# Kernel tuning notes

Hardware: AMD Instinct MI355X
Metric: run time of the kernel (lower is better)

Reference implementation:

```python
import jax, jax.numpy as jnp
import numpy as np

DISTANCE_SCALE = 25.0
VIEW_PE = 6
STEP = 0.02  # nominal ray-march step size used to scale dists


def positional_encoding(positions, freqs):
    # matches torch: (positions[..., None] * 2**k).reshape(..., freqs*C) -> [sin, cos]
    freq_bands = 2.0 ** jnp.arange(freqs, dtype=positions.dtype)
    pts = (positions[..., None] * freq_bands).reshape(positions.shape[:-1] + (freqs * positions.shape[-1],))
    return jnp.concatenate([jnp.sin(pts), jnp.cos(pts)], axis=-1)


def setup_inputs() -> dict:
    key = jax.random.key(0)
    ks = jax.random.split(key, 10)
    n_rays, n_samples, C, featureC = 4096, 256, 27, 128
    in_mlpC = 3 + 2 * VIEW_PE * 3 + C  # 66
    density_features = jax.random.normal(ks[0], (n_rays, n_samples), jnp.float32)
    app_features = jax.random.normal(ks[1], (n_rays, n_samples, C), jnp.float32)
    viewdirs = jax.random.normal(ks[2], (n_rays, 3), jnp.float32)
    viewdirs = viewdirs / jnp.linalg.norm(viewdirs, axis=-1, keepdims=True)
    dists = jax.random.uniform(ks[3], (n_rays, n_samples), jnp.float32) * STEP
    s1 = 1.0 / np.sqrt(in_mlpC)
    s2 = 1.0 / np.sqrt(featureC)
    W1 = jax.random.uniform(ks[4], (in_mlpC, featureC), jnp.float32, -s1, s1)
    b1 = jax.random.uniform(ks[5], (featureC,), jnp.float32, -s1, s1)
    W2 = jax.random.uniform(ks[6], (featureC, featureC), jnp.float32, -s2, s2)
    b2 = jax.random.uniform(ks[7], (featureC,), jnp.float32, -s2, s2)
    W3 = jax.random.uniform(ks[8], (featureC, 3), jnp.float32, -s2, s2)
    b3 = jnp.zeros((3,), jnp.float32)  # torch init: constant_(bias, 0)
    return {"density_features": density_features, "app_features": app_features,
            "viewdirs": viewdirs, "dists": dists,
            "W1": W1, "b1": b1, "W2": W2, "b2": b2, "W3": W3, "b3": b3}


def reference(density_features, app_features, viewdirs, dists, W1, b1, W2, b2, W3, b3):
    # feature2density (relu activation)
    sigma = jax.nn.relu(density_features)  # [R, S]
    # raw2alpha
    alpha = 1.0 - jnp.exp(-sigma * dists * DISTANCE_SCALE)  # [R, S]
    T = jnp.cumprod(jnp.concatenate([jnp.ones((alpha.shape[0], 1), alpha.dtype),
                                     1.0 - alpha + 1e-10], axis=-1), axis=-1)
    weights = alpha * T[:, :-1]  # [R, S]
    # radiance MLP over all sample points
    R, S, C = app_features.shape
    vd = jnp.broadcast_to(viewdirs[:, None, :], (R, S, 3))
    mlp_in = jnp.concatenate([app_features, vd, positional_encoding(vd, VIEW_PE)], axis=-1)  # [R,S,66]
    h = jax.nn.relu(mlp_in @ W1 + b1)
    h = jax.nn.relu(h @ W2 + b2)
    rgb = jax.nn.sigmoid(h @ W3 + b3)  # [R, S, 3]
    # composite (white background)
    acc_map = jnp.sum(weights, axis=-1)  # [R]
    rgb_map = jnp.einsum('rs,rsc->rc', weights, rgb)  # [R, 3]
    rgb_map = jnp.clip(rgb_map + (1.0 - acc_map[:, None]), 0.0, 1.0)
    return rgb_map
```

## Files before the change

### kernel.cpp

```cpp
#include <hip/hip_runtime.h>
#include <hip/hip_bf16.h>

typedef float f32x4 __attribute__((ext_vector_type(4)));
typedef short s16x8 __attribute__((ext_vector_type(8)));
typedef unsigned int u32;
typedef u32 u32x2 __attribute__((ext_vector_type(2)));

#define DIST_SCALE 25.0f

__device__ __forceinline__ unsigned short f2b(float f) {
  union { float f; unsigned u; } v; v.f = f;
  unsigned r = v.u + 0x7fffu + ((v.u >> 16) & 1u);
  return (unsigned short)(r >> 16);
}

__device__ __forceinline__ u32 cvtpk(float lo, float hi) {
  u32 r;
  asm("v_cvt_pk_bf16_f32 %0, %1, %2" : "=v"(r) : "v"(lo), "v"(hi));
  return r;
}

__device__ __forceinline__ int swzH(int s, int chbyte) {
  return (s * 256 + chbyte) ^ ((s & 7) << 4);
}

__global__ void prep_weights(const float* __restrict__ W1, const float* __restrict__ W2,
                             const float* __restrict__ W3, unsigned short* __restrict__ ws) {
  int t = blockIdx.x * 256 + threadIdx.x;
  int stride = gridDim.x * 256;
  for (int i = t; i < 128 * 32; i += stride) {
    int n = i >> 5, k = i & 31;
    ws[i] = (k < 27) ? f2b(W1[k * 128 + n]) : (unsigned short)0;
  }
  unsigned short* w2t = ws + 4096;
  for (int i = t; i < 128 * 128; i += stride) {
    int n = i >> 7, k = i & 127;
    w2t[i] = f2b(W2[k * 128 + n]);
  }
  unsigned short* w3p = ws + 4096 + 16384;
  for (int i = t; i < 4 * 16 * 32; i += stride) {
    int wv = i >> 9, rem = i & 511, n = rem >> 5, ks = rem & 31;
    int kg = ks >> 3, j = ks & 7;
    int ch = wv * 32 + ((j >> 2) << 4) + kg * 4 + (j & 3);
    w3p[i] = (n < 3) ? f2b(W3[ch * 3 + n]) : (unsigned short)0;
  }
}

__global__ void __launch_bounds__(256, 3) nerf_main(
    const float* __restrict__ dens, const float* __restrict__ app,
    const float* __restrict__ vdirs, const float* __restrict__ dists,
    const float* __restrict__ W1, const float* __restrict__ b1,
    const float* __restrict__ b2v, const float* __restrict__ b3v,
    const unsigned short* __restrict__ wsb, float* __restrict__ out) {
  __shared__ unsigned short Xs[64 * 40];
  __shared__ unsigned short HA[64 * 128];
  __shared__ float part[4 * 64 * 3];
  __shared__ float wbuf[256];
  __shared__ float hcbuf[128];
  __shared__ float featbuf[40];
  __shared__ float red[4][4];

  const int t = threadIdx.x;
  const int lane = t & 63;
  const int wv = t >> 6;
  const int r = blockIdx.x;

  const unsigned short* W1aT = wsb;
  const unsigned short* W2T = wsb + 4096;
  const unsigned short* W3P = wsb + 4096 + 16384;
  char* HAb = (char*)HA;

  const int cl = lane & 15;
  const int kg = lane >> 4;
  const int chBase = wv * 32;

  for (int i = t; i < 1280; i += 256) ((u32*)Xs)[i] = 0u;
  if (t < 39) {
    float val;
    if (t < 3) val = vdirs[r * 3 + t];
    else {
      int jj = t - 3;
      int trig = jj / 18;
      int rem = jj % 18;
      int c = rem / 6, k = rem % 6;
      float v = vdirs[r * 3 + c] * (float)(1 << k);
      val = trig ? cosf(v) : sinf(v);
    }
    featbuf[t] = val;
  }
  if (wv == 0) {
    const float4 dv = *(const float4*)(dens + (size_t)r * 256 + lane * 4);
    const float4 tv = *(const float4*)(dists + (size_t)r * 256 + lane * 4);
    float f[4], al[4];
    float dl[4] = {dv.x, dv.y, dv.z, dv.w};
    float tl[4] = {tv.x, tv.y, tv.z, tv.w};
    float p = 1.0f;
#pragma unroll
    for (int q = 0; q < 4; ++q) {
      float sg = fmaxf(dl[q], 0.0f);
      float e = __expf(-sg * tl[q] * DIST_SCALE);
      al[q] = 1.0f - e;
      f[q] = e + 1e-10f;
      p *= f[q];
    }
    float P = p;
#pragma unroll
    for (int dlt = 1; dlt < 64; dlt <<= 1) {
      float v = __shfl_up(P, dlt, 64);
      if (lane >= dlt) P *= v;
    }
    float E = __shfl_up(P, 1, 64);
    if (lane == 0) E = 1.0f;
    float tr = E;
#pragma unroll
    for (int q = 0; q < 4; ++q) { wbuf[lane * 4 + q] = al[q] * tr; tr *= f[q]; }
  }
  __syncthreads();
  if (t < 128) {
    float s = b1[t];
    for (int j = 0; j < 39; ++j) s += featbuf[j] * W1[(27 + j) * 128 + t];
    hcbuf[t] = s;
  }

  s16x8 w1f[2], w2f[2][4], w3s;
#pragma unroll
  for (int nt = 0; nt < 2; ++nt)
    w1f[nt] = *(const s16x8*)(W1aT + (chBase + nt * 16 + cl) * 32 + kg * 8);
#pragma unroll
  for (int nt = 0; nt < 2; ++nt)
#pragma unroll
    for (int kk = 0; kk < 4; ++kk)
      w2f[nt][kk] = *(const s16x8*)(W2T + (chBase + nt * 16 + cl) * 128 + kk * 32 + kg * 8);
  w3s = *(const s16x8*)(W3P + wv * 512 + cl * 32 + kg * 8);

  __syncthreads();

  float pr = 0.0f, pg = 0.0f, pb = 0.0f, pw = 0.0f;
  const float b30 = b3v[0], b31 = b3v[1], b32 = b3v[2];
  const f32x4 hc0 = *(const f32x4*)(hcbuf + chBase + kg * 4);
  const f32x4 hc1 = *(const f32x4*)(hcbuf + chBase + 16 + kg * 4);
  const f32x4 bb0 = *(const f32x4*)(b2v + chBase + kg * 4);
  const f32x4 bb1 = *(const f32x4*)(b2v + chBase + 16 + kg * 4);

  const float* rayBase = app + (size_t)r * 256 * 27;
  f32x4 L0 = *(const f32x4*)(rayBase + 4 * t);
  f32x4 L1 = {};
  if (t < 176) L1 = *(const f32x4*)(rayBase + 4 * (t + 256));

  for (int chunk = 0; chunk < 4; ++chunk) {
    const int sBase = chunk * 64;
    {
      unsigned e0 = 4u * (unsigned)t;
      unsigned s0 = e0 / 27u, c0 = e0 - s0 * 27u;
      unsigned base = s0 * 80u + 2u * c0;
#pragma unroll
      for (int u2 = 0; u2 < 4; ++u2) {
        unsigned a = base + 2u * u2 + ((c0 + u2 >= 27u) ? 26u : 0u);
        *(unsigned short*)((char*)Xs + a) = f2b(L0[u2]);
      }
      if (t < 176) {
        unsigned e1 = 4u * (unsigned)(t + 256);
        unsigned s1 = e1 / 27u, c1 = e1 - s1 * 27u;
        unsigned bs1 = s1 * 80u + 2u * c1;
#pragma unroll
        for (int u2 = 0; u2 < 4; ++u2) {
          unsigned a = bs1 + 2u * u2 + ((c1 + u2 >= 27u) ? 26u : 0u);
          *(unsigned short*)((char*)Xs + a) = f2b(L1[u2]);
        }
      }
    }
    __syncthreads();

    if (chunk < 3) {
      const float* slab = rayBase + (size_t)(chunk + 1) * 1728;
      L0 = *(const f32x4*)(slab + 4 * t);
      if (t < 176) L1 = *(const f32x4*)(slab + 4 * (t + 256));
    }

#pragma unroll
    for (int st = 0; st < 4; ++st) {
      const int s = st * 16 + cl;
      s16x8 xb = *(const s16x8*)((char*)Xs + s * 80 + kg * 16);
      f32x4 a0 = hc0, a1 = hc1;
      a0 = __builtin_amdgcn_mfma_f32_16x16x32_bf16(w1f[0], xb, a0, 0, 0, 0);
      a1 = __builtin_amdgcn_mfma_f32_16x16x32_bf16(w1f[1], xb, a1, 0, 0, 0);
      u32x2 pk0 = {cvtpk(fmaxf(a0[0], 0.0f), fmaxf(a0[1], 0.0f)),
                   cvtpk(fmaxf(a0[2], 0.0f), fmaxf(a0[3], 0.0f))};
      u32x2 pk1 = {cvtpk(fmaxf(a1[0], 0.0f), fmaxf(a1[1], 0.0f)),
                   cvtpk(fmaxf(a1[2], 0.0f), fmaxf(a1[3], 0.0f))};
      *(u32x2*)(HAb + swzH(s, (chBase + kg * 4) * 2)) = pk0;
      *(u32x2*)(HAb + swzH(s, (chBase + 16 + kg * 4) * 2)) = pk1;
    }
    __syncthreads();

#pragma unroll
    for (int st = 0; st < 4; ++st) {
      const int s = st * 16 + cl;
      s16x8 hbf[4];
#pragma unroll
      for (int kk = 0; kk < 4; ++kk)
        hbf[kk] = *(const s16x8*)(HAb + swzH(s, (kk * 32 + kg * 8) * 2));
      f32x4 a0 = bb0, a1 = bb1;
#pragma unroll
      for (int kk = 0; kk < 4; ++kk) {
        a0 = __builtin_amdgcn_mfma_f32_16x16x32_bf16(w2f[0][kk], hbf[kk], a0, 0, 0, 0);
        a1 = __builtin_amdgcn_mfma_f32_16x16x32_bf16(w2f[1][kk], hbf[kk], a1, 0, 0, 0);
      }
      union { u32 u[4]; s16x8 v; } b3;
      b3.u[0] = cvtpk(fmaxf(a0[0], 0.0f), fmaxf(a0[1], 0.0f));
      b3.u[1] = cvtpk(fmaxf(a0[2], 0.0f), fmaxf(a0[3], 0.0f));
      b3.u[2] = cvtpk(fmaxf(a1[0], 0.0f), fmaxf(a1[1], 0.0f));
      b3.u[3] = cvtpk(fmaxf(a1[2], 0.0f), fmaxf(a1[3], 0.0f));
      f32x4 p3 = {};
      p3 = __builtin_amdgcn_mfma_f32_16x16x32_bf16(w3s, b3.v, p3, 0, 0, 0);
      if (kg == 0) {
        float* pp = part + (wv * 64 + s) * 3;
        pp[0] = p3[0]; pp[1] = p3[1]; pp[2] = p3[2];
      }
    }
    __syncthreads();

    {
      const float* pp = part + ((kg * 64) + wv * 16 + cl) * 3;
      float v0 = pp[0], v1 = pp[1], v2 = pp[2];
      v0 += __shfl_xor(v0, 16, 64); v0 += __shfl_xor(v0, 32, 64);
      v1 += __shfl_xor(v1, 16, 64); v1 += __shfl_xor(v1, 32, 64);
      v2 += __shfl_xor(v2, 16, 64); v2 += __shfl_xor(v2, 32, 64);
      if (kg == 0) {
        float w = wbuf[sBase + wv * 16 + cl];
        pw += w;
        pr += w / (1.0f + __expf(-(v0 + b30)));
        pg += w / (1.0f + __expf(-(v1 + b31)));
        pb += w / (1.0f + __expf(-(v2 + b32)));
      }
    }
  }

  if (kg == 0) {
#pragma unroll
    for (int d = 1; d < 16; d <<= 1) {
      pr += __shfl_xor(pr, d, 64);
      pg += __shfl_xor(pg, d, 64);
      pb += __shfl_xor(pb, d, 64);
      pw += __shfl_xor(pw, d, 64);
    }
    if (lane == 0) { red[wv][0] = pr; red[wv][1] = pg; red[wv][2] = pb; red[wv][3] = pw; }
  }
  __syncthreads();
  if (t == 0) {
    float R = 0, G = 0, B = 0, W = 0;
#pragma unroll
    for (int w = 0; w < 4; ++w) { R += red[w][0]; G += red[w][1]; B += red[w][2]; W += red[w][3]; }
    float bg = 1.0f - W;
    out[r * 3 + 0] = fminf(fmaxf(R + bg, 0.0f), 1.0f);
    out[r * 3 + 1] = fminf(fmaxf(G + bg, 0.0f), 1.0f);
    out[r * 3 + 2] = fminf(fmaxf(B + bg, 0.0f), 1.0f);
  }
}

extern "C" void kernel_launch(void* const* d_in, const int* in_sizes, int n_in,
                              void* d_out, int out_size, void* d_ws, size_t ws_size,
                              hipStream_t stream) {
  const float* dens = (const float*)d_in[0];
  const float* app  = (const float*)d_in[1];
  const float* vd   = (const float*)d_in[2];
  const float* dist = (const float*)d_in[3];
  const float* W1   = (const float*)d_in[4];
  const float* b1   = (const float*)d_in[5];
  const float* W2   = (const float*)d_in[6];
  const float* b2   = (const float*)d_in[7];
  const float* W3   = (const float*)d_in[8];
  const float* b3   = (const float*)d_in[9];
  unsigned short* wsb = (unsigned short*)d_ws;

  prep_weights<<<32, 256, 0, stream>>>(W1, W2, W3, wsb);
  nerf_main<<<4096, 256, 0, stream>>>(dens, app, vd, dist, W1, b1, b2, b3, wsb, (float*)d_out);
}
```

Baseline: 81.67 us.

## Load app features straight into MFMA fragments and fold epilogue reduction across lanes

Drops the LDS staging buffer for the per-chunk app feature slab. Each lane now reads its 8 floats directly from global memory and packs them to bf16 in registers for the first-layer MFMA. This removes one barrier per chunk and the scattered 16-bit LDS stores. Lanes reading past channel 27 pick up values from the next sample, which assumes the padded W1 rows are zero; the last ray's final chunk gets a guard to avoid reading out of bounds. The epilogue is also reorganised so the four lane groups each handle one of R, G, B and the weight sum, with a transposed partial buffer, and LDS is merged into a smaller pool. The explicit next-chunk prefetch is gone, so global load latency now sits directly ahead of the MFMAs.

```diff
diff --git a/kernel.cpp b/kernel.cpp
--- a/kernel.cpp
+++ b/kernel.cpp
@@ -52,12 +52,9 @@
     const float* __restrict__ W1, const float* __restrict__ b1,
     const float* __restrict__ b2v, const float* __restrict__ b3v,
     const unsigned short* __restrict__ wsb, float* __restrict__ out) {
-  __shared__ unsigned short Xs[64 * 40];
   __shared__ unsigned short HA[64 * 128];
-  __shared__ float part[4 * 64 * 3];
+  __shared__ __align__(16) float pool[768];
   __shared__ float wbuf[256];
-  __shared__ float hcbuf[128];
-  __shared__ float featbuf[40];
   __shared__ float red[4][4];
 
   const int t = threadIdx.x;
@@ -73,8 +70,9 @@
   const int cl = lane & 15;
   const int kg = lane >> 4;
   const int chBase = wv * 32;
-
-  for (int i = t; i < 1280; i += 256) ((u32*)Xs)[i] = 0u;
+  float* featbuf = pool;
+  float* hcbuf = pool + 64;
+
   if (t < 39) {
     float val;
     if (t < 3) val = vdirs[r * 3 + t];
@@ -134,56 +132,46 @@
   w3s = *(const s16x8*)(W3P + wv * 512 + cl * 32 + kg * 8);
 
   __syncthreads();
-
-  float pr = 0.0f, pg = 0.0f, pb = 0.0f, pw = 0.0f;
-  const float b30 = b3v[0], b31 = b3v[1], b32 = b3v[2];
   const f32x4 hc0 = *(const f32x4*)(hcbuf + chBase + kg * 4);
   const f32x4 hc1 = *(const f32x4*)(hcbuf + chBase + 16 + kg * 4);
   const f32x4 bb0 = *(const f32x4*)(b2v + chBase + kg * 4);
   const f32x4 bb1 = *(const f32x4*)(b2v + chBase + 16 + kg * 4);
-
-  const float* rayBase = app + (size_t)r * 256 * 27;
-  f32x4 L0 = *(const f32x4*)(rayBase + 4 * t);
-  f32x4 L1 = {};
-  if (t < 176) L1 = *(const f32x4*)(rayBase + 4 * (t + 256));
+  const float b3c = (kg < 3) ? b3v[kg] : 0.0f;
+  float pacc = 0.0f;
+  float* part = pool;
+
+  const float* rayBase = app + (size_t)r * 6912;
 
   for (int chunk = 0; chunk < 4; ++chunk) {
     const int sBase = chunk * 64;
-    {
-      unsigned e0 = 4u * (unsigned)t;
-      unsigned s0 = e0 / 27u, c0 = e0 - s0 * 27u;
-      unsigned base = s0 * 80u + 2u * c0;
-#pragma unroll
-      for (int u2 = 0; u2 < 4; ++u2) {
-        unsigned a = base + 2u * u2 + ((c0 + u2 >= 27u) ? 26u : 0u);
-        *(unsigned short*)((char*)Xs + a) = f2b(L0[u2]);
-      }
-      if (t < 176) {
-        unsigned e1 = 4u * (unsigned)(t + 256);
-        unsigned s1 = e1 / 27u, c1 = e1 - s1 * 27u;
-        unsigned bs1 = s1 * 80u + 2u * c1;
-#pragma unroll
-        for (int u2 = 0; u2 < 4; ++u2) {
-          unsigned a = bs1 + 2u * u2 + ((c1 + u2 >= 27u) ? 26u : 0u);
-          *(unsigned short*)((char*)Xs + a) = f2b(L1[u2]);
-        }
-      }
-    }
-    __syncthreads();
-
-    if (chunk < 3) {
-      const float* slab = rayBase + (size_t)(chunk + 1) * 1728;
-      L0 = *(const f32x4*)(slab + 4 * t);
-      if (t < 176) L1 = *(const f32x4*)(slab + 4 * (t + 256));
-    }
+    const float* ckBase = rayBase + chunk * 1728;
+    const bool tailCk = (r == 4095) && (chunk == 3);
 
 #pragma unroll
     for (int st = 0; st < 4; ++st) {
       const int s = st * 16 + cl;
-      s16x8 xb = *(const s16x8*)((char*)Xs + s * 80 + kg * 16);
+      const float* gp = ckBase + s * 27 + kg * 8;
+      f32x4 va, vb;
+      if (__builtin_expect(tailCk && st == 3, 0)) {
+        if (kg == 3 && cl == 15) {
+          va = (f32x4){gp[0], gp[1], gp[2], 0.0f};
+          vb = (f32x4){0.0f, 0.0f, 0.0f, 0.0f};
+        } else {
+          va = *(const f32x4*)gp;
+          vb = *(const f32x4*)(gp + 4);
+        }
+      } else {
+        va = *(const f32x4*)gp;
+        vb = *(const f32x4*)(gp + 4);
+      }
+      union { u32 u[4]; s16x8 v; } xb;
+      xb.u[0] = cvtpk(va[0], va[1]);
+      xb.u[1] = cvtpk(va[2], va[3]);
+      xb.u[2] = cvtpk(vb[0], vb[1]);
+      xb.u[3] = cvtpk(vb[2], vb[3]);
       f32x4 a0 = hc0, a1 = hc1;
-      a0 = __builtin_amdgcn_mfma_f32_16x16x32_bf16(w1f[0], xb, a0, 0, 0, 0);
-      a1 = __builtin_amdgcn_mfma_f32_16x16x32_bf16(w1f[1], xb, a1, 0, 0, 0);
+      a0 = __builtin_amdgcn_mfma_f32_16x16x32_bf16(w1f[0], xb.v, a0, 0, 0, 0);
+      a1 = __builtin_amdgcn_mfma_f32_16x16x32_bf16(w1f[1], xb.v, a1, 0, 0, 0);
       u32x2 pk0 = {cvtpk(fmaxf(a0[0], 0.0f), fmaxf(a0[1], 0.0f)),
                    cvtpk(fmaxf(a0[2], 0.0f), fmaxf(a0[3], 0.0f))};
       u32x2 pk1 = {cvtpk(fmaxf(a1[0], 0.0f), fmaxf(a1[1], 0.0f)),
@@ -214,43 +202,36 @@
       f32x4 p3 = {};
       p3 = __builtin_amdgcn_mfma_f32_16x16x32_bf16(w3s, b3.v, p3, 0, 0, 0);
       if (kg == 0) {
-        float* pp = part + (wv * 64 + s) * 3;
-        pp[0] = p3[0]; pp[1] = p3[1]; pp[2] = p3[2];
+        float* pp = part + s * 12;
+        pp[wv] = p3[0];
+        pp[4 + wv] = p3[1];
+        pp[8 + wv] = p3[2];
       }
     }
     __syncthreads();
 
     {
-      const float* pp = part + ((kg * 64) + wv * 16 + cl) * 3;
-      float v0 = pp[0], v1 = pp[1], v2 = pp[2];
-      v0 += __shfl_xor(v0, 16, 64); v0 += __shfl_xor(v0, 32, 64);
-      v1 += __shfl_xor(v1, 16, 64); v1 += __shfl_xor(v1, 32, 64);
-      v2 += __shfl_xor(v2, 16, 64); v2 += __shfl_xor(v2, 32, 64);
-      if (kg == 0) {
-        float w = wbuf[sBase + wv * 16 + cl];
-        pw += w;
-        pr += w / (1.0f + __expf(-(v0 + b30)));
-        pg += w / (1.0f + __expf(-(v1 + b31)));
-        pb += w / (1.0f + __expf(-(v2 + b32)));
-      }
-    }
-  }
-
-  if (kg == 0) {
-#pragma unroll
-    for (int d = 1; d < 16; d <<= 1) {
-      pr += __shfl_xor(pr, d, 64);
-      pg += __shfl_xor(pg, d, 64);
-      pb += __shfl_xor(pb, d, 64);
-      pw += __shfl_xor(pw, d, 64);
-    }
-    if (lane == 0) { red[wv][0] = pr; red[wv][1] = pg; red[wv][2] = pb; red[wv][3] = pw; }
-  }
+      const int s = wv * 16 + cl;
+      const float w = wbuf[sBase + s];
+      if (kg < 3) {
+        f32x4 pv = *(const f32x4*)(part + s * 12 + kg * 4);
+        float v = (pv[0] + pv[1]) + (pv[2] + pv[3]) + b3c;
+        pacc += w / (1.0f + __expf(-v));
+      } else {
+        pacc += w;
+      }
+    }
+  }
+
+#pragma unroll
+  for (int d = 1; d < 16; d <<= 1) pacc += __shfl_xor(pacc, d, 64);
+  if (cl == 0) red[wv][kg] = pacc;
   __syncthreads();
   if (t == 0) {
-    float R = 0, G = 0, B = 0, W = 0;
-#pragma unroll
-    for (int w = 0; w < 4; ++w) { R += red[w][0]; G += red[w][1]; B += red[w][2]; W += red[w][3]; }
+    float R = red[0][0] + red[1][0] + red[2][0] + red[3][0];
+    float G = red[0][1] + red[1][1] + red[2][1] + red[3][1];
+    float B = red[0][2] + red[1][2] + red[2][2] + red[3][2];
+    float W = red[0][3] + red[1][3] + red[2][3] + red[3][3];
     float bg = 1.0f - W;
     out[r * 3 + 0] = fminf(fmaxf(R + bg, 0.0f), 1.0f);
     out[r * 3 + 1] = fminf(fmaxf(G + bg, 0.0f), 1.0f);
```

Result: slower. 94.34 us (+15.5%).
